# Kernel optimization log

Measured on AMD Instinct MI355X. Metric: run time of the kernel, lower is better.

Reference implementation:

```python
import jax, jax.numpy as jnp
import numpy as np

EPS = 1e-08


def setup_inputs() -> dict:
    key = jax.random.key(0)
    k1, k2 = jax.random.split(key)
    batch, num_experts, d_model = 16384, 8, 512
    expert_states = jax.random.normal(k1, (batch, num_experts, d_model), dtype=jnp.float32)
    # module initializes this param to 0.01; use small random values around that scale
    nonlocal_correlation = 0.01 * jax.random.normal(k2, (num_experts, num_experts), dtype=jnp.float32)
    return {"expert_states": expert_states, "nonlocal_correlation": nonlocal_correlation}


def reference(expert_states, nonlocal_correlation):
    E = nonlocal_correlation.shape[0]
    # entangled[b,i] = x[b,i] + sum_{j!=i} sigmoid(corr[i,j]) * x[b,j]
    W = jax.nn.sigmoid(nonlocal_correlation) * (1.0 - jnp.eye(E, dtype=expert_states.dtype))
    entangled = expert_states + jnp.einsum('ij,bjd->bid', W, expert_states)
    # concurrence: trace(entangled[0] @ entangled[0]^T) = sum of squares of entangled[0]
    D = entangled.shape[-1]
    trace0 = jnp.sum(entangled[0] * entangled[0])
    measure = jnp.abs(trace0) / (E * D + EPS)
    return (entangled, measure)
```

## Files before the change

### kernel.cpp

```cpp
#include <hip/hip_runtime.h>
#include <math.h>

#define NE 8
#define ND 512
#define NB 16384
#define DV (ND / 4)
#define EPSF 1e-8f

__global__ void prep_M(const float* __restrict__ corr, float* __restrict__ M) {
    int t = threadIdx.x;
    if (t < NE * NE) {
        int i = t >> 3, j = t & 7;
        float s = 1.0f / (1.0f + expf(-corr[t]));
        M[t] = (i == j) ? 1.0f : s;
    }
}

__global__ __launch_bounds__(256) void entangle(const float4* __restrict__ x,
                                                const float* __restrict__ M,
                                                float4* __restrict__ out) {
    __shared__ float sM[NE * NE];
    if (threadIdx.x < NE * NE) sM[threadIdx.x] = M[threadIdx.x];
    __syncthreads();

    int tid = blockIdx.x * blockDim.x + threadIdx.x;
    int b  = tid >> 7;
    int dv = tid & (DV - 1);
    long base = (long)b * (NE * DV) + dv;

    float4 xv[NE];
#pragma unroll
    for (int j = 0; j < NE; ++j) xv[j] = x[base + j * DV];

#pragma unroll
    for (int i = 0; i < NE; ++i) {
        float4 acc = make_float4(0.f, 0.f, 0.f, 0.f);
#pragma unroll
        for (int j = 0; j < NE; ++j) {
            float m = sM[i * NE + j];
            acc.x = fmaf(m, xv[j].x, acc.x);
            acc.y = fmaf(m, xv[j].y, acc.y);
            acc.z = fmaf(m, xv[j].z, acc.z);
            acc.w = fmaf(m, xv[j].w, acc.w);
        }
        out[base + i * DV] = acc;
    }
}

__global__ __launch_bounds__(256) void measure_k(const float4* __restrict__ ent,
                                                 float* __restrict__ out_measure) {
    float s = 0.f;
    for (int k = threadIdx.x; k < NE * DV; k += 256) {
        float4 v = ent[k];
        s += v.x * v.x + v.y * v.y + v.z * v.z + v.w * v.w;
    }
#pragma unroll
    for (int off = 32; off > 0; off >>= 1) s += __shfl_down(s, off);
    __shared__ float ws[4];
    int lane = threadIdx.x & 63, w = threadIdx.x >> 6;
    if (lane == 0) ws[w] = s;
    __syncthreads();
    if (threadIdx.x == 0) {
        float t = ws[0] + ws[1] + ws[2] + ws[3];
        out_measure[0] = fabsf(t) / ((float)(NE * ND) + EPSF);
    }
}

extern "C" void kernel_launch(void* const* d_in, const int* in_sizes, int n_in,
                              void* d_out, int out_size, void* d_ws, size_t ws_size,
                              hipStream_t stream) {
    const float* x    = (const float*)d_in[0];
    const float* corr = (const float*)d_in[1];
    float* out = (float*)d_out;
    float* M   = (float*)d_ws;

    prep_M<<<1, 64, 0, stream>>>(corr, M);

    int total_threads = NB * DV;
    entangle<<<total_threads / 256, 256, 0, stream>>>(
        (const float4*)x, M, (float4*)out);

    measure_k<<<1, 256, 0, stream>>>((const float4*)out,
                                     out + (size_t)NB * NE * ND);
}
```

Baseline: 109.2 us.

## Fuse sigmoid prep, entangle and measure into one kernel with nontemporal IO

Combines the three launches into one kernel. Each block computes the sigmoid mixing matrix into shared memory, and block 0 reduces the sum of squares of batch row 0 on the fly instead of re-reading it in a separate launch. Global loads and stores are now nontemporal hints. This removes two launches and their serialization gaps, at the cost of every block redoing the 64 sigmoid evaluations.

```diff
diff --git a/kernel.cpp b/kernel.cpp
--- a/kernel.cpp
+++ b/kernel.cpp
@@ -5,64 +5,58 @@
 #define ND 512
 #define NB 16384
 #define DV (ND / 4)
-#define EPSF 1e-8f
 
-__global__ void prep_M(const float* __restrict__ corr, float* __restrict__ M) {
-    int t = threadIdx.x;
-    if (t < NE * NE) {
-        int i = t >> 3, j = t & 7;
-        float s = 1.0f / (1.0f + expf(-corr[t]));
-        M[t] = (i == j) ? 1.0f : s;
+typedef float f32x4 __attribute__((ext_vector_type(4)));
+
+__global__ __launch_bounds__(256) void fused_entangle(
+        const f32x4* __restrict__ x,
+        const float* __restrict__ corr,
+        f32x4*       __restrict__ out,
+        float*       __restrict__ measure_out) {
+    __shared__ float sM[NE * NE];
+    if (threadIdx.x < NE * NE) {
+        int i = threadIdx.x >> 3, j = threadIdx.x & 7;
+        float c = corr[threadIdx.x];
+        float s = 1.0f / (1.0f + expf(-c));
+        sM[threadIdx.x] = (i == j) ? 1.0f : s;
     }
-}
-
-__global__ __launch_bounds__(256) void entangle(const float4* __restrict__ x,
-                                                const float* __restrict__ M,
-                                                float4* __restrict__ out) {
-    __shared__ float sM[NE * NE];
-    if (threadIdx.x < NE * NE) sM[threadIdx.x] = M[threadIdx.x];
     __syncthreads();
 
-    int tid = blockIdx.x * blockDim.x + threadIdx.x;
+    int tid = blockIdx.x * 256 + threadIdx.x;
     int b  = tid >> 7;
-    int dv = tid & (DV - 1);
-    long base = (long)b * (NE * DV) + dv;
+    long base = (long)b * (NE * DV) + (tid & (DV - 1));
 
-    float4 xv[NE];
+    f32x4 xv[NE];
 #pragma unroll
-    for (int j = 0; j < NE; ++j) xv[j] = x[base + j * DV];
+    for (int j = 0; j < NE; ++j)
+        xv[j] = __builtin_nontemporal_load(&x[base + j * DV]);
 
+    float ssq = 0.f;
 #pragma unroll
     for (int i = 0; i < NE; ++i) {
-        float4 acc = make_float4(0.f, 0.f, 0.f, 0.f);
+        f32x4 acc = (f32x4)(0.f);
 #pragma unroll
         for (int j = 0; j < NE; ++j) {
             float m = sM[i * NE + j];
-            acc.x = fmaf(m, xv[j].x, acc.x);
-            acc.y = fmaf(m, xv[j].y, acc.y);
-            acc.z = fmaf(m, xv[j].z, acc.z);
-            acc.w = fmaf(m, xv[j].w, acc.w);
+            acc = xv[j] * m + acc;
         }
-        out[base + i * DV] = acc;
+        __builtin_nontemporal_store(acc, &out[base + i * DV]);
+        if (b == 0)
+            ssq += acc.x * acc.x + acc.y * acc.y + acc.z * acc.z + acc.w * acc.w;
     }
-}
 
-__global__ __launch_bounds__(256) void measure_k(const float4* __restrict__ ent,
-                                                 float* __restrict__ out_measure) {
-    float s = 0.f;
-    for (int k = threadIdx.x; k < NE * DV; k += 256) {
-        float4 v = ent[k];
-        s += v.x * v.x + v.y * v.y + v.z * v.z + v.w * v.w;
-    }
+    if (blockIdx.x == 0) {
 #pragma unroll
-    for (int off = 32; off > 0; off >>= 1) s += __shfl_down(s, off);
-    __shared__ float ws[4];
-    int lane = threadIdx.x & 63, w = threadIdx.x >> 6;
-    if (lane == 0) ws[w] = s;
-    __syncthreads();
-    if (threadIdx.x == 0) {
-        float t = ws[0] + ws[1] + ws[2] + ws[3];
-        out_measure[0] = fabsf(t) / ((float)(NE * ND) + EPSF);
+        for (int off = 32; off > 0; off >>= 1)
+            ssq += __shfl_down(ssq, off);
+        __shared__ float ws[4];
+        int lane = threadIdx.x & 63, w = threadIdx.x >> 6;
+        if (lane == 0) ws[w] = ssq;
+        __syncthreads();
+        if (threadIdx.x == 0) {
+            float t = ws[0] + ws[1] + ws[2] + ws[3];
+            measure_out[0] = fabsf(t) / ((float)(NE * ND) + 1e-8f);
+        }
     }
 }
 
@@ -72,14 +66,9 @@
     const float* x    = (const float*)d_in[0];
     const float* corr = (const float*)d_in[1];
     float* out = (float*)d_out;
-    float* M   = (float*)d_ws;
-
-    prep_M<<<1, 64, 0, stream>>>(corr, M);
 
     int total_threads = NB * DV;
-    entangle<<<total_threads / 256, 256, 0, stream>>>(
-        (const float4*)x, M, (float4*)out);
-
-    measure_k<<<1, 256, 0, stream>>>((const float4*)out,
-                                     out + (size_t)NB * NE * ND);
+    fused_entangle<<<total_threads / 256, 256, 0, stream>>>(
+        (const f32x4*)x, corr, (f32x4*)out,
+        out + (size_t)NB * NE * ND);
 }
```

Result: faster. 92.24 us (-15.6%).
